# Kernel tuning notes

Hardware: AMD Instinct MI355X
Metric: run time of the kernel (lower is better)

The kernel has to match this reference:

```python
import jax, jax.numpy as jnp
import numpy as np

# ---- fixed encoding config (mirrors PermutoEncoding __init__ args) ----
POS_DIM = 3
DP1 = POS_DIM + 1                 # simplex has pos_dim+1 vertices
CAPACITY = 262144                 # hash table size per level (2^18)
NR_LEVELS = 24
NR_FEAT = 2
N_POINTS = 262144
SCALES = np.geomspace(1.0, 1e-4, NR_LEVELS).astype(np.float32)  # coarse -> fine
# permutohedral elevation scale factors (Adams et al.): 1/sqrt((i+1)(i+2)) * invStdDev
INV_STD_DEV = DP1 * np.sqrt(2.0 / 3.0)
SCALE_FACTOR = (INV_STD_DEV / np.sqrt((np.arange(POS_DIM) + 1.0) * (np.arange(POS_DIM) + 2.0))).astype(np.float32)
PRIMES = np.array([2654435761, 805459861, 3674653429], dtype=np.uint32)


def setup_inputs() -> dict:
    key = jax.random.key(0)
    k1, k2, k3 = jax.random.split(key, 3)
    positions = jax.random.uniform(k1, (N_POINTS, POS_DIM), jnp.float32)
    # matches torch.randn(capacity, L, F)*1e-5 permuted to [L, C, F]
    lattice_values = jax.random.normal(k2, (NR_LEVELS, CAPACITY, NR_FEAT), jnp.float32) * 1e-5
    random_shift = jax.random.normal(k3, (NR_LEVELS, POS_DIM), jnp.float32) * 10.0
    anneal_window = jnp.ones((NR_LEVELS,), jnp.float32)
    return {"positions": positions, "lattice_values": lattice_values,
            "random_shift": random_shift, "anneal_window": anneal_window}


def _permuto_encode(positions, lattice_values, random_shift, anneal_window):
    scales = jnp.asarray(SCALES)
    sf = jnp.asarray(SCALE_FACTOR)
    # per-level scaled + shifted positions: [L, N, d]
    p = positions[None, :, :] / scales[:, None, None] + random_shift[:, None, :]
    cf = p * sf                                              # [L,N,d]
    # elevate onto hyperplane H_d in R^{d+1}
    rev_cumsum = jnp.cumsum(cf[..., ::-1], axis=-1)[..., ::-1]   # S[k] = sum_{j>=k} cf[j]
    e0 = rev_cumsum[..., :1]                                 # elevated[0] = sum cf
    S = jnp.concatenate([rev_cumsum[..., 1:], jnp.zeros_like(e0)], axis=-1)
    irange = jnp.arange(1, DP1, dtype=cf.dtype)
    elevated = jnp.concatenate([e0, S - irange * cf], axis=-1)  # [L,N,d+1]

    # nearest zero-colored lattice point (round each coord to multiple of d+1)
    rem0 = jnp.round(elevated / DP1) * DP1                   # [L,N,d+1]
    dvec = elevated - rem0
    # rank[i] = #{j>i : d_i < d_j} + #{j<i : d_j >= d_i}
    less = dvec[..., :, None] < dvec[..., None, :]           # [.., i, j] = d_i < d_j
    idxr = jnp.arange(DP1)
    j_gt_i = idxr[:, None] < idxr[None, :]
    j_lt_i = idxr[:, None] > idxr[None, :]
    rank = (less & j_gt_i).sum(-1).astype(jnp.int32) \
         + ((~jnp.swapaxes(less, -1, -2)) & j_lt_i).sum(-1).astype(jnp.int32)
    s = jnp.round(rem0.sum(-1) / DP1).astype(jnp.int32)      # [L,N]
    rank = rank + s[..., None]
    lo = rank < 0
    rank = rank + lo.astype(jnp.int32) * DP1
    rem0 = rem0 + lo.astype(rem0.dtype) * DP1
    hi = rank > POS_DIM
    rank = rank - hi.astype(jnp.int32) * DP1
    rem0 = rem0 - hi.astype(rem0.dtype) * DP1

    # barycentric weights (size d+2, wrapped)
    delta = (elevated - rem0) / DP1
    oh = jax.nn.one_hot(POS_DIM - rank, DP1 + 1, dtype=delta.dtype) \
       - jax.nn.one_hot(DP1 - rank, DP1 + 1, dtype=delta.dtype)
    b = jnp.einsum('...i,...ij->...j', delta, oh)            # [L,N,d+2]
    w0 = b[..., 0] + 1.0 + b[..., DP1]
    weights = jnp.concatenate([w0[..., None], b[..., 1:DP1]], axis=-1)  # [L,N,d+1]

    # simplex vertex keys (first d coords), one per remainder r=0..d
    r = jnp.arange(DP1, dtype=jnp.int32)                     # vertex axis
    rem0i = jnp.round(rem0).astype(jnp.int32)
    keys = rem0i[..., None, :POS_DIM] + r[:, None] \
         - DP1 * (rank[..., None, :POS_DIM] > POS_DIM - r[:, None]).astype(jnp.int32)  # [L,N,d+1,d]

    # hash keys into the per-level table
    ku = keys.astype(jnp.uint32) * jnp.asarray(PRIMES)[None, None, None, :]
    h = ku[..., 0] ^ ku[..., 1] ^ ku[..., 2]
    idx = (h % jnp.uint32(CAPACITY)).astype(jnp.int32)       # [L,N,d+1]

    # gather per-level features and blend with barycentric weights
    vals = jax.vmap(lambda tbl, ix: tbl[ix])(lattice_values, idx)   # [L,N,d+1,F]
    sliced = jnp.einsum('lnv,lnvf->lnf', weights, vals) * anneal_window[:, None, None]
    # (L,F,N).permute(2,0,1).reshape(N,-1) == [N, L, F] -> [N, L*F]
    return jnp.transpose(sliced, (1, 0, 2)).reshape(positions.shape[0], -1)


def reference(positions, lattice_values, random_shift, anneal_window):
    return _permuto_encode(positions, lattice_values, random_shift, anneal_window)
```

## Files before the change

### kernel.cpp

```cpp
#include <hip/hip_runtime.h>
#include <math.h>

#define N_LEVELS 24
#define CAPACITY 262144u
#define CAP_MASK 0x3FFFFu

struct ScaleArg { float s[N_LEVELS]; };

__device__ __forceinline__ float2 permuto_level(
    float p0, float p1, float p2,
    float scale, float s0, float s1, float s2,
    const float2* __restrict__ tab )
{
#pragma clang fp contract(off)
    const float sf0 = 2.3094010767585034f;
    const float sf1 = 1.3333333333333335f;
    const float sf2 = 0.9428090415820634f;

    const float q0 = p0 / scale + s0;
    const float q1 = p1 / scale + s1;
    const float q2 = p2 / scale + s2;
    const float cf0 = q0 * sf0;
    const float cf1 = q1 * sf1;
    const float cf2 = q2 * sf2;

    const float rc1 = cf2 + cf1;
    const float el0 = rc1 + cf0;
    const float el1 = rc1 - cf0;
    const float el2 = cf2 - 2.0f * cf1;
    const float el3 = 0.0f - 3.0f * cf2;

    float r0 = rintf(el0 * 0.25f) * 4.0f;
    float r1 = rintf(el1 * 0.25f) * 4.0f;
    float r2 = rintf(el2 * 0.25f) * 4.0f;
    float r3 = rintf(el3 * 0.25f) * 4.0f;

    const float d0 = el0 - r0;
    const float d1 = el1 - r1;
    const float d2 = el2 - r2;
    const float d3 = el3 - r3;

    int k0 = 0, k1 = 0, k2 = 0, k3 = 0;
    if (d0 < d1) k0++; else k1++;
    if (d0 < d2) k0++; else k2++;
    if (d0 < d3) k0++; else k3++;
    if (d1 < d2) k1++; else k2++;
    if (d1 < d3) k1++; else k3++;
    if (d2 < d3) k2++; else k3++;

    const int s = (int)rintf((((r0 + r1) + r2) + r3) * 0.25f);
    k0 += s; k1 += s; k2 += s; k3 += s;

    if (k0 < 0) { k0 += 4; r0 += 4.0f; } else if (k0 > 3) { k0 -= 4; r0 -= 4.0f; }
    if (k1 < 0) { k1 += 4; r1 += 4.0f; } else if (k1 > 3) { k1 -= 4; r1 -= 4.0f; }
    if (k2 < 0) { k2 += 4; r2 += 4.0f; } else if (k2 > 3) { k2 -= 4; r2 -= 4.0f; }
    if (k3 < 0) { k3 += 4; r3 += 4.0f; } else if (k3 > 3) { k3 -= 4; r3 -= 4.0f; }

    const float dl0 = (el0 - r0) * 0.25f;
    const float dl1 = (el1 - r1) * 0.25f;
    const float dl2 = (el2 - r2) * 0.25f;
    const float dl3 = (el3 - r3) * 0.25f;

    const float g0 = (k0 == 0 ? dl0 : 0.0f) + (k1 == 0 ? dl1 : 0.0f) + (k2 == 0 ? dl2 : 0.0f) + (k3 == 0 ? dl3 : 0.0f);
    const float g1 = (k0 == 1 ? dl0 : 0.0f) + (k1 == 1 ? dl1 : 0.0f) + (k2 == 1 ? dl2 : 0.0f) + (k3 == 1 ? dl3 : 0.0f);
    const float g2 = (k0 == 2 ? dl0 : 0.0f) + (k1 == 2 ? dl1 : 0.0f) + (k2 == 2 ? dl2 : 0.0f) + (k3 == 2 ? dl3 : 0.0f);
    const float g3 = (k0 == 3 ? dl0 : 0.0f) + (k1 == 3 ? dl1 : 0.0f) + (k2 == 3 ? dl2 : 0.0f) + (k3 == 3 ? dl3 : 0.0f);

    const float w0 = g3 + 1.0f - g0;
    const float w1 = g2 - g3;
    const float w2 = g1 - g2;
    const float w3 = g0 - g1;

    const int i0 = (int)r0;
    const int i1 = (int)r1;
    const int i2 = (int)r2;

    float acc0 = 0.0f, acc1 = 0.0f;
#pragma unroll
    for (int r = 0; r < 4; ++r) {
        const int key0 = i0 + r - ((k0 > 3 - r) ? 4 : 0);
        const int key1 = i1 + r - ((k1 > 3 - r) ? 4 : 0);
        const int key2 = i2 + r - ((k2 > 3 - r) ? 4 : 0);
        const unsigned hsh = (unsigned)key0 * 2654435761u
                           ^ (unsigned)key1 * 805459861u
                           ^ (unsigned)key2 * 3674653429u;
        const float2 v = tab[hsh & CAP_MASK];
        const float w = (r == 0) ? w0 : (r == 1) ? w1 : (r == 2) ? w2 : w3;
        acc0 += w * v.x;
        acc1 += w * v.y;
    }
    return make_float2(acc0, acc1);
}

__global__ __launch_bounds__(256)
void permuto_gather(const float* __restrict__ pos,
                    const float* __restrict__ lattice,
                    const float* __restrict__ rshift,
                    const float* __restrict__ anneal,
                    float2* __restrict__ ws,
                    ScaleArg sc, int npts, int chunksPerLevel)
{
#pragma clang fp contract(off)
    const int i = blockIdx.x;
    const int xcd = i & 7;
    const int j = i >> 3;
    const int phase = j / chunksPerLevel;
    const int chunk = j - phase * chunksPerLevel;
    const int level = phase * 8 + xcd;

    const int n = chunk * 256 + threadIdx.x;
    if (n >= npts) return;

    const float scale = sc.s[level];
    const float s0 = rshift[level * 3 + 0];
    const float s1 = rshift[level * 3 + 1];
    const float s2 = rshift[level * 3 + 2];
    const float a  = anneal[level];

    const float p0 = pos[n * 3 + 0];
    const float p1 = pos[n * 3 + 1];
    const float p2 = pos[n * 3 + 2];

    const float2* tab = (const float2*)lattice + (size_t)level * CAPACITY;
    float2 acc = permuto_level(p0, p1, p2, scale, s0, s1, s2, tab);
    ws[(size_t)level * npts + n] = make_float2(acc.x * a, acc.y * a);
}

__global__ __launch_bounds__(256)
void permuto_transpose(const float2* __restrict__ ws,
                       float4* __restrict__ out, int npts)
{
    const int n = blockIdx.x * 256 + threadIdx.x;
    if (n >= npts) return;
    float2 v[N_LEVELS];
#pragma unroll
    for (int l = 0; l < N_LEVELS; ++l)
        v[l] = ws[(size_t)l * npts + n];
    float4* o = out + (size_t)n * (N_LEVELS / 2);
#pragma unroll
    for (int k = 0; k < N_LEVELS / 2; ++k)
        o[k] = make_float4(v[2 * k].x, v[2 * k].y, v[2 * k + 1].x, v[2 * k + 1].y);
}

__global__ __launch_bounds__(256)
void permuto_mono(const float* __restrict__ pos,
                  const float* __restrict__ lattice,
                  const float* __restrict__ rshift,
                  const float* __restrict__ anneal,
                  float* __restrict__ out,
                  ScaleArg sc, int npts)
{
#pragma clang fp contract(off)
    __shared__ float sh_shift[N_LEVELS][3];
    __shared__ float sh_ann[N_LEVELS];
    const int tid = threadIdx.x;
    if (tid < N_LEVELS) {
        sh_shift[tid][0] = rshift[tid * 3 + 0];
        sh_shift[tid][1] = rshift[tid * 3 + 1];
        sh_shift[tid][2] = rshift[tid * 3 + 2];
        sh_ann[tid] = anneal[tid];
    }
    __syncthreads();

    const int n = blockIdx.x * 256 + tid;
    if (n >= npts) return;
    const float p0 = pos[n * 3 + 0];
    const float p1 = pos[n * 3 + 1];
    const float p2 = pos[n * 3 + 2];
    float2* outv = (float2*)out + (size_t)n * N_LEVELS;
    for (int l = 0; l < N_LEVELS; ++l) {
        const float2* tab = (const float2*)lattice + (size_t)l * CAPACITY;
        float2 acc = permuto_level(p0, p1, p2, sc.s[l],
                                   sh_shift[l][0], sh_shift[l][1], sh_shift[l][2], tab);
        outv[l] = make_float2(acc.x * sh_ann[l], acc.y * sh_ann[l]);
    }
}

extern "C" void kernel_launch(void* const* d_in, const int* in_sizes, int n_in,
                              void* d_out, int out_size, void* d_ws, size_t ws_size,
                              hipStream_t stream) {
    const float* pos     = (const float*)d_in[0];
    const float* lattice = (const float*)d_in[1];
    const float* rshift  = (const float*)d_in[2];
    const float* anneal  = (const float*)d_in[3];
    const int npts = in_sizes[0] / 3;

    ScaleArg sc;
    for (int i = 0; i < N_LEVELS; ++i)
        sc.s[i] = (float)pow(10.0, (double)i * (-4.0 / 23.0));
    sc.s[0] = 1.0f;
    sc.s[N_LEVELS - 1] = 1e-4f;

    const size_t ws_need = (size_t)N_LEVELS * (size_t)npts * sizeof(float2);
    if (ws_size >= ws_need) {
        const int C = (npts + 255) / 256;
        const int blocks1 = 8 * 3 * C;
        permuto_gather<<<blocks1, 256, 0, stream>>>(
            pos, lattice, rshift, anneal, (float2*)d_ws, sc, npts, C);
        const int blocks2 = (npts + 255) / 256;
        permuto_transpose<<<blocks2, 256, 0, stream>>>(
            (const float2*)d_ws, (float4*)d_out, npts);
    } else {
        const int blocks = (npts + 255) / 256;
        permuto_mono<<<blocks, 256, 0, stream>>>(
            pos, lattice, rshift, anneal, (float*)d_out, sc, npts);
    }
}
```

Baseline: 244.9 us.

## Process four points per thread in gather and stage transpose through shared memory

The gather kernel now has each thread handle four consecutive points. Positions are read with vectorized float4 loads, all 16 table gathers are issued before any accumulation, and results are written as float4. The aim is more memory-level parallelism and fewer narrow loads and stores. The transpose kernel now stages the 24 level rows in padded shared memory so that global writes of the interleaved output are coalesced rather than strided 192 bytes per thread. In exchange the gather launches a quarter as many threads, raises register pressure, and changes summation order in the weighted blend.

```diff
diff --git a/kernel.cpp b/kernel.cpp
--- a/kernel.cpp
+++ b/kernel.cpp
@@ -7,10 +7,14 @@
 
 struct ScaleArg { float s[N_LEVELS]; };
 
-__device__ __forceinline__ float2 permuto_level(
+struct Prep {
+    float w0, w1, w2, w3;
+    unsigned i0, i1, i2, i3;
+};
+
+__device__ __forceinline__ Prep permuto_prep(
     float p0, float p1, float p2,
-    float scale, float s0, float s1, float s2,
-    const float2* __restrict__ tab )
+    float scale, float s0, float s1, float s2)
 {
 #pragma clang fp contract(off)
     const float sf0 = 2.3094010767585034f;
@@ -66,16 +70,17 @@
     const float g2 = (k0 == 2 ? dl0 : 0.0f) + (k1 == 2 ? dl1 : 0.0f) + (k2 == 2 ? dl2 : 0.0f) + (k3 == 2 ? dl3 : 0.0f);
     const float g3 = (k0 == 3 ? dl0 : 0.0f) + (k1 == 3 ? dl1 : 0.0f) + (k2 == 3 ? dl2 : 0.0f) + (k3 == 3 ? dl3 : 0.0f);
 
-    const float w0 = g3 + 1.0f - g0;
-    const float w1 = g2 - g3;
-    const float w2 = g1 - g2;
-    const float w3 = g0 - g1;
+    Prep out;
+    out.w0 = g3 + 1.0f - g0;
+    out.w1 = g2 - g3;
+    out.w2 = g1 - g2;
+    out.w3 = g0 - g1;
 
     const int i0 = (int)r0;
     const int i1 = (int)r1;
     const int i2 = (int)r2;
 
-    float acc0 = 0.0f, acc1 = 0.0f;
+    unsigned idx[4];
 #pragma unroll
     for (int r = 0; r < 4; ++r) {
         const int key0 = i0 + r - ((k0 > 3 - r) ? 4 : 0);
@@ -84,21 +89,19 @@
         const unsigned hsh = (unsigned)key0 * 2654435761u
                            ^ (unsigned)key1 * 805459861u
                            ^ (unsigned)key2 * 3674653429u;
-        const float2 v = tab[hsh & CAP_MASK];
-        const float w = (r == 0) ? w0 : (r == 1) ? w1 : (r == 2) ? w2 : w3;
-        acc0 += w * v.x;
-        acc1 += w * v.y;
-    }
-    return make_float2(acc0, acc1);
+        idx[r] = hsh & CAP_MASK;
+    }
+    out.i0 = idx[0]; out.i1 = idx[1]; out.i2 = idx[2]; out.i3 = idx[3];
+    return out;
 }
 
 __global__ __launch_bounds__(256)
-void permuto_gather(const float* __restrict__ pos,
-                    const float* __restrict__ lattice,
-                    const float* __restrict__ rshift,
-                    const float* __restrict__ anneal,
-                    float2* __restrict__ ws,
-                    ScaleArg sc, int npts, int chunksPerLevel)
+void permuto_gather4(const float* __restrict__ pos,
+                     const float* __restrict__ lattice,
+                     const float* __restrict__ rshift,
+                     const float* __restrict__ anneal,
+                     float2* __restrict__ ws,
+                     ScaleArg sc, int npts, int chunksPerLevel)
 {
 #pragma clang fp contract(off)
     const int i = blockIdx.x;
@@ -108,8 +111,8 @@
     const int chunk = j - phase * chunksPerLevel;
     const int level = phase * 8 + xcd;
 
-    const int n = chunk * 256 + threadIdx.x;
-    if (n >= npts) return;
+    const int base = chunk * 1024 + threadIdx.x * 4;
+    if (base >= npts) return;
 
     const float scale = sc.s[level];
     const float s0 = rshift[level * 3 + 0];
@@ -117,29 +120,95 @@
     const float s2 = rshift[level * 3 + 2];
     const float a  = anneal[level];
 
-    const float p0 = pos[n * 3 + 0];
-    const float p1 = pos[n * 3 + 1];
-    const float p2 = pos[n * 3 + 2];
-
-    const float2* tab = (const float2*)lattice + (size_t)level * CAPACITY;
-    float2 acc = permuto_level(p0, p1, p2, scale, s0, s1, s2, tab);
-    ws[(size_t)level * npts + n] = make_float2(acc.x * a, acc.y * a);
+    const float2* __restrict__ tab = (const float2*)lattice + (size_t)level * CAPACITY;
+    float2* __restrict__ wrow = ws + (size_t)level * npts;
+
+    if (base + 3 < npts) {
+        const float4* pv = (const float4*)(pos + (size_t)base * 3);
+        const float4 f0 = pv[0];
+        const float4 f1 = pv[1];
+        const float4 f2 = pv[2];
+        const float px[4] = { f0.x, f0.w, f1.z, f2.y };
+        const float py[4] = { f0.y, f1.x, f1.w, f2.z };
+        const float pz[4] = { f0.z, f1.y, f2.x, f2.w };
+
+        Prep pr[4];
+#pragma unroll
+        for (int k = 0; k < 4; ++k)
+            pr[k] = permuto_prep(px[k], py[k], pz[k], scale, s0, s1, s2);
+
+        float2 v[4][4];
+#pragma unroll
+        for (int k = 0; k < 4; ++k) {
+            v[k][0] = tab[pr[k].i0];
+            v[k][1] = tab[pr[k].i1];
+            v[k][2] = tab[pr[k].i2];
+            v[k][3] = tab[pr[k].i3];
+        }
+
+        float2 acc[4];
+#pragma unroll
+        for (int k = 0; k < 4; ++k) {
+            float ax = pr[k].w0 * v[k][0].x + pr[k].w1 * v[k][1].x
+                     + pr[k].w2 * v[k][2].x + pr[k].w3 * v[k][3].x;
+            float ay = pr[k].w0 * v[k][0].y + pr[k].w1 * v[k][1].y
+                     + pr[k].w2 * v[k][2].y + pr[k].w3 * v[k][3].y;
+            acc[k] = make_float2(ax * a, ay * a);
+        }
+
+        float4* o = (float4*)(wrow + base);
+        o[0] = make_float4(acc[0].x, acc[0].y, acc[1].x, acc[1].y);
+        o[1] = make_float4(acc[2].x, acc[2].y, acc[3].x, acc[3].y);
+    } else {
+        for (int k = 0; k < 4 && base + k < npts; ++k) {
+            const int n = base + k;
+            Prep pr = permuto_prep(pos[n * 3 + 0], pos[n * 3 + 1], pos[n * 3 + 2],
+                                   scale, s0, s1, s2);
+            float2 v0 = tab[pr.i0], v1 = tab[pr.i1], v2 = tab[pr.i2], v3 = tab[pr.i3];
+            float ax = pr.w0 * v0.x + pr.w1 * v1.x + pr.w2 * v2.x + pr.w3 * v3.x;
+            float ay = pr.w0 * v0.y + pr.w1 * v1.y + pr.w2 * v2.y + pr.w3 * v3.y;
+            wrow[n] = make_float2(ax * a, ay * a);
+        }
+    }
 }
 
 __global__ __launch_bounds__(256)
 void permuto_transpose(const float2* __restrict__ ws,
                        float4* __restrict__ out, int npts)
 {
-    const int n = blockIdx.x * 256 + threadIdx.x;
-    if (n >= npts) return;
-    float2 v[N_LEVELS];
-#pragma unroll
-    for (int l = 0; l < N_LEVELS; ++l)
-        v[l] = ws[(size_t)l * npts + n];
-    float4* o = out + (size_t)n * (N_LEVELS / 2);
-#pragma unroll
-    for (int k = 0; k < N_LEVELS / 2; ++k)
-        o[k] = make_float4(v[2 * k].x, v[2 * k].y, v[2 * k + 1].x, v[2 * k + 1].y);
+    __shared__ float2 sh[N_LEVELS][257];
+    const int t = threadIdx.x;
+    const int pbase = blockIdx.x * 256;
+    const int valid = npts - pbase;
+
+    if (valid >= 256) {
+#pragma unroll
+        for (int l = 0; l < N_LEVELS; ++l)
+            sh[l][t] = ws[(size_t)l * npts + pbase + t];
+        __syncthreads();
+
+        float4* o = out + (size_t)pbase * 12;
+#pragma unroll
+        for (int s = 0; s < 12; ++s) {
+            const int q = s * 256 + t;
+            const int p = q / 12;
+            const int j = q - p * 12;
+            const float2 va = sh[2 * j][p];
+            const float2 vb = sh[2 * j + 1][p];
+            o[q] = make_float4(va.x, va.y, vb.x, vb.y);
+        }
+    } else {
+        if (t < valid) {
+            const int n = pbase + t;
+            float4* o = out + (size_t)n * 12;
+#pragma unroll
+            for (int j = 0; j < 12; ++j) {
+                const float2 va = ws[(size_t)(2 * j) * npts + n];
+                const float2 vb = ws[(size_t)(2 * j + 1) * npts + n];
+                o[j] = make_float4(va.x, va.y, vb.x, vb.y);
+            }
+        }
+    }
 }
 
 __global__ __launch_bounds__(256)
@@ -170,9 +239,12 @@
     float2* outv = (float2*)out + (size_t)n * N_LEVELS;
     for (int l = 0; l < N_LEVELS; ++l) {
         const float2* tab = (const float2*)lattice + (size_t)l * CAPACITY;
-        float2 acc = permuto_level(p0, p1, p2, sc.s[l],
-                                   sh_shift[l][0], sh_shift[l][1], sh_shift[l][2], tab);
-        outv[l] = make_float2(acc.x * sh_ann[l], acc.y * sh_ann[l]);
+        Prep pr = permuto_prep(p0, p1, p2, sc.s[l],
+                               sh_shift[l][0], sh_shift[l][1], sh_shift[l][2]);
+        float2 v0 = tab[pr.i0], v1 = tab[pr.i1], v2 = tab[pr.i2], v3 = tab[pr.i3];
+        float ax = pr.w0 * v0.x + pr.w1 * v1.x + pr.w2 * v2.x + pr.w3 * v3.x;
+        float ay = pr.w0 * v0.y + pr.w1 * v1.y + pr.w2 * v2.y + pr.w3 * v3.y;
+        outv[l] = make_float2(ax * sh_ann[l], ay * sh_ann[l]);
     }
 }
 
@@ -193,9 +265,9 @@
 
     const size_t ws_need = (size_t)N_LEVELS * (size_t)npts * sizeof(float2);
     if (ws_size >= ws_need) {
-        const int C = (npts + 255) / 256;
+        const int C = (npts + 1023) / 1024;
         const int blocks1 = 8 * 3 * C;
-        permuto_gather<<<blocks1, 256, 0, stream>>>(
+        permuto_gather4<<<blocks1, 256, 0, stream>>>(
             pos, lattice, rshift, anneal, (float2*)d_ws, sc, npts, C);
         const int blocks2 = (npts + 255) / 256;
         permuto_transpose<<<blocks2, 256, 0, stream>>>(
```

After: 211.1 us. 1.16x faster.
